# Performance work log

Measured on AMD Instinct MI355X. Metric: run time of the kernel, lower is better.

## Reference

```python
import jax, jax.numpy as jnp
import numpy as np

EPS = 1e-6

def _rms(x, w):
    # RMSNorm over last dim with learned scale w
    var = jnp.mean(x * x, axis=-1, keepdims=True)
    return x * jax.lax.rsqrt(var + EPS) * w

def _split_heads(x, h):
    b, l, hd = x.shape
    return x.reshape(b, l, h, hd // h).transpose(0, 2, 1, 3)  # b h l d

def setup_inputs() -> dict:
    key = jax.random.key(0)
    ks = jax.random.split(key, 12)
    D = 2048          # hidden_size == ip_hidden_states_dim
    H = 16            # n_heads
    Dh = 128          # head_dim
    T = 1280          # timesteps_emb_dim
    B, L, Lip = 2, 2048, 512
    s = 0.02
    return {
        "ip_hidden_states": jax.random.normal(ks[0], (B, Lip, D), jnp.float32),
        "img_query": jax.random.normal(ks[1], (B, L, D), jnp.float32),
        "img_key": jax.random.normal(ks[2], (B, L, D), jnp.float32),
        "img_value": jax.random.normal(ks[3], (B, L, D), jnp.float32),
        "t_emb": jax.random.normal(ks[4], (B, T), jnp.float32),
        "W_ada": jax.random.normal(ks[5], (2 * D, T), jnp.float32) * s,
        "b_ada": jax.random.normal(ks[6], (2 * D,), jnp.float32) * s,
        "W_k_ip": jax.random.normal(ks[7], (D, D), jnp.float32) * s,
        "W_v_ip": jax.random.normal(ks[8], (D, D), jnp.float32) * s,
        "w_q": jnp.ones((Dh,), jnp.float32),
        "w_k": jnp.ones((Dh,), jnp.float32),
        "w_ipk": jnp.ones((Dh,), jnp.float32),
        "n_heads": H,
    }

def reference(ip_hidden_states, img_query, img_key, img_value, t_emb,
              W_ada, b_ada, W_k_ip, W_v_ip, w_q, w_k, w_ipk, n_heads):
    D = img_query.shape[-1]
    # AdaLayerNorm (mode='normal'): silu -> linear -> shift/scale, LN(no affine)
    emb = jax.nn.silu(t_emb) @ W_ada.T + b_ada          # [B, 2D]
    shift, scale = emb[:, :D], emb[:, D:]
    x = ip_hidden_states
    mu = jnp.mean(x, axis=-1, keepdims=True)
    var = jnp.mean((x - mu) ** 2, axis=-1, keepdims=True)
    xn = (x - mu) * jax.lax.rsqrt(var + 1e-6)
    ip_n = xn * (1.0 + scale[:, None, :]) + shift[:, None, :]
    # K/V projections for IP tokens
    ip_key = ip_n @ W_k_ip.T
    ip_value = ip_n @ W_v_ip.T
    # split heads
    q = _split_heads(img_query, n_heads)   # b h L d
    k = _split_heads(img_key, n_heads)
    v = _split_heads(img_value, n_heads)
    kip = _split_heads(ip_key, n_heads)    # b h Lip d
    vip = _split_heads(ip_value, n_heads)
    # RMSNorms
    q = _rms(q, w_q)
    k = _rms(k, w_k)
    kip = _rms(kip, w_ipk)
    # concat image + IP along sequence
    kcat = jnp.concatenate([k, kip], axis=2)
    vcat = jnp.concatenate([v, vip], axis=2)
    # SDPA
    d = q.shape[-1]
    scores = jnp.einsum('bhld,bhmd->bhlm', q, kcat) / jnp.sqrt(jnp.asarray(d, q.dtype))
    attn = jax.nn.softmax(scores, axis=-1)
    out = jnp.einsum('bhlm,bhmd->bhld', attn, vcat)
    b, h, l, dh = out.shape
    return out.transpose(0, 2, 1, 3).reshape(b, l, h * dh)
```

## Files before the change

kernel.cpp:

```cpp
#include <hip/hip_runtime.h>
#include <hip/hip_bf16.h>

typedef __attribute__((ext_vector_type(8))) __bf16 bf16x8;
typedef __attribute__((ext_vector_type(2))) __bf16 bf16x2;
typedef __attribute__((ext_vector_type(4))) float floatx4;
typedef __attribute__((ext_vector_type(4))) short short4v;

#define DEV static __device__ __forceinline__

typedef __attribute__((address_space(1))) const unsigned int gu32;
typedef __attribute__((address_space(3))) unsigned int lu32;

DEV void dma16(const void* g, void* l) {
  __builtin_amdgcn_global_load_lds((gu32*)g, (lu32*)l, 16, 0, 0);
}

DEV unsigned short f2bf(float f) {
  unsigned int u = __float_as_uint(f);
  u += 0x7fffu + ((u >> 16) & 1u);
  return (unsigned short)(u >> 16);
}

DEV unsigned int pk_bf16(float a, float b) {
#if __has_builtin(__builtin_amdgcn_cvt_pk_bf16_f32)
  bf16x2 r = __builtin_amdgcn_cvt_pk_bf16_f32(a, b);
  union { bf16x2 v; unsigned int u; } c; c.v = r;
  return c.u;
#else
  return (unsigned int)f2bf(a) | ((unsigned int)f2bf(b) << 16);
#endif
}

DEV float wred_sum(float v) {
#pragma unroll
  for (int o = 32; o > 0; o >>= 1) v += __shfl_xor(v, o, 64);
  return v;
}

DEV floatx4 mfma32(bf16x8 a, bf16x8 b, floatx4 c) {
  return __builtin_amdgcn_mfma_f32_16x16x32_bf16(a, b, c, 0, 0, 0);
}
DEV floatx4 mfma16(short4v a, short4v b, floatx4 c) {
  return __builtin_amdgcn_mfma_f32_16x16x16bf16_1k(a, b, c, 0, 0, 0);
}

__global__ void ada_kernel(const float* __restrict__ t_emb, const float* __restrict__ W_ada,
                           const float* __restrict__ b_ada, float* __restrict__ emb) {
  int w = threadIdx.x >> 6, lane = threadIdx.x & 63;
  int gid = blockIdx.x * 4 + w;
  int b = gid >> 12, n = gid & 4095;
  const float* te = t_emb + (size_t)b * 1280;
  const float* wr = W_ada + (size_t)n * 1280;
  float acc = 0.f;
#pragma unroll
  for (int i = 0; i < 20; ++i) {
    int t = lane + i * 64;
    float x = te[t];
    float s = x / (1.f + __expf(-x));
    acc += s * wr[t];
  }
  acc = wred_sum(acc);
  if (lane == 0) emb[gid] = acc + b_ada[n];
}

__global__ void ln_mod_kernel(const float* __restrict__ ip, const float* __restrict__ emb,
                              unsigned short* __restrict__ ipn) {
  int row = blockIdx.x;
  int b = row >> 9;
  const float* x = ip + (size_t)row * 2048;
  float xv[8];
  float s1 = 0.f, s2 = 0.f;
#pragma unroll
  for (int i = 0; i < 8; ++i) {
    float v = x[threadIdx.x + i * 256];
    xv[i] = v; s1 += v; s2 += v * v;
  }
  s1 = wred_sum(s1); s2 = wred_sum(s2);
  __shared__ float r1[4], r2[4];
  int w = threadIdx.x >> 6, lane = threadIdx.x & 63;
  if (lane == 0) { r1[w] = s1; r2[w] = s2; }
  __syncthreads();
  s1 = r1[0] + r1[1] + r1[2] + r1[3];
  s2 = r2[0] + r2[1] + r2[2] + r2[3];
  float mu = s1 * (1.f / 2048.f);
  float var = s2 * (1.f / 2048.f) - mu * mu;
  float rs = rsqrtf(var + 1e-6f);
  const float* sh = emb + (size_t)b * 4096;
  unsigned short* y = ipn + (size_t)row * 2048;
#pragma unroll
  for (int i = 0; i < 8; ++i) {
    int d = threadIdx.x + i * 256;
    float v = (xv[i] - mu) * rs;
    v = v * (1.f + sh[2048 + d]) + sh[d];
    y[d] = f2bf(v);
  }
}

struct us4 { unsigned short a, b, c, d; };
__global__ void cvtw_kernel(const float* __restrict__ wk, const float* __restrict__ wv,
                            unsigned short* __restrict__ wk16, unsigned short* __restrict__ wv16) {
  size_t i = ((size_t)blockIdx.x * 256 + threadIdx.x) * 4;
  float4 a = *(const float4*)(wk + i);
  float4 b = *(const float4*)(wv + i);
  us4 oa = { f2bf(a.x), f2bf(a.y), f2bf(a.z), f2bf(a.w) };
  us4 ob = { f2bf(b.x), f2bf(b.y), f2bf(b.z), f2bf(b.w) };
  *(us4*)(wk16 + i) = oa;
  *(us4*)(wv16 + i) = ob;
}

__global__ __launch_bounds__(256) void proj_gemm(const unsigned short* __restrict__ A,
    const unsigned short* __restrict__ Wk, const unsigned short* __restrict__ Wv,
    float* __restrict__ Ck, float* __restrict__ Cv) {
  const unsigned short* Bm = blockIdx.z ? Wv : Wk;
  float* C = blockIdx.z ? Cv : Ck;
  int n0 = blockIdx.x * 64, m0 = blockIdx.y * 128;
  __shared__ __align__(16) unsigned short As[128 * 72];
  __shared__ __align__(16) unsigned short Bs[64 * 72];
  int tid = threadIdx.x, w = tid >> 6, lane = tid & 63, quad = lane >> 4, l16 = lane & 15;
  floatx4 acc[2][4];
#pragma unroll
  for (int i = 0; i < 2; ++i)
#pragma unroll
    for (int j = 0; j < 4; ++j) { floatx4 z = {0.f, 0.f, 0.f, 0.f}; acc[i][j] = z; }
  for (int kk = 0; kk < 2048; kk += 64) {
#pragma unroll
    for (int it = 0; it < 4; ++it) {
      int idx = tid + it * 256;
      int row = idx >> 3, chk = idx & 7;
      *(uint4*)&As[row * 72 + chk * 8] = *(const uint4*)&A[(size_t)(m0 + row) * 2048 + kk + chk * 8];
    }
#pragma unroll
    for (int it = 0; it < 2; ++it) {
      int idx = tid + it * 256;
      int row = idx >> 3, chk = idx & 7;
      *(uint4*)&Bs[row * 72 + chk * 8] = *(const uint4*)&Bm[(size_t)(n0 + row) * 2048 + kk + chk * 8];
    }
    __syncthreads();
#pragma unroll
    for (int c = 0; c < 2; ++c) {
      bf16x8 a0 = *(const bf16x8*)&As[(w * 32 + l16) * 72 + quad * 8 + c * 32];
      bf16x8 a1 = *(const bf16x8*)&As[(w * 32 + 16 + l16) * 72 + quad * 8 + c * 32];
#pragma unroll
      for (int nt = 0; nt < 4; ++nt) {
        bf16x8 bb = *(const bf16x8*)&Bs[(nt * 16 + l16) * 72 + quad * 8 + c * 32];
        acc[0][nt] = mfma32(a0, bb, acc[0][nt]);
        acc[1][nt] = mfma32(a1, bb, acc[1][nt]);
      }
    }
    __syncthreads();
  }
#pragma unroll
  for (int rt = 0; rt < 2; ++rt)
#pragma unroll
    for (int nt = 0; nt < 4; ++nt)
#pragma unroll
      for (int r = 0; r < 4; ++r)
        C[(size_t)(m0 + w * 32 + rt * 16 + quad * 4 + r) * 2048 + n0 + nt * 16 + l16] = acc[rt][nt][r];
}

__global__ __launch_bounds__(256) void kv_build(const float* __restrict__ img_key, const float* __restrict__ img_value,
                         const float* __restrict__ ipk, const float* __restrict__ ipv,
                         const float* __restrict__ w_k, const float* __restrict__ w_ipk,
                         unsigned short* __restrict__ Kc, unsigned short* __restrict__ VtT) {
  int bh = blockIdx.x;
  int mt = blockIdx.y;
  int b = bh >> 4, hh = bh & 15;
  int m0 = mt * 64;
  __shared__ __align__(16) unsigned short Vs[64 * 132];
  int tid = threadIdx.x;
  int mrow = tid >> 2, dq = tid & 3;
  int m = m0 + mrow;
  size_t base;
  const float* wsrc;
  const float *ksrc, *vsrc;
  if (m < 2048) {
    base = (size_t)(b * 2048 + m) * 2048 + hh * 128;
    ksrc = img_key + base; vsrc = img_value + base; wsrc = w_k;
  } else {
    base = (size_t)(b * 512 + (m - 2048)) * 2048 + hh * 128;
    ksrc = ipk + base; vsrc = ipv + base; wsrc = w_ipk;
  }
  float kvv[32]; float ss = 0.f;
  const float4* k4 = (const float4*)ksrc;
#pragma unroll
  for (int i = 0; i < 8; ++i) {
    float4 x = k4[dq * 8 + i];
    kvv[i * 4 + 0] = x.x; kvv[i * 4 + 1] = x.y; kvv[i * 4 + 2] = x.z; kvv[i * 4 + 3] = x.w;
    ss += x.x * x.x + x.y * x.y + x.z * x.z + x.w * x.w;
  }
  ss += __shfl_xor(ss, 1, 64);
  ss += __shfl_xor(ss, 2, 64);
  float rs = rsqrtf(ss * (1.f / 128.f) + 1e-6f);
  unsigned short kb[32];
#pragma unroll
  for (int j = 0; j < 32; ++j) kb[j] = f2bf(kvv[j] * rs * wsrc[dq * 32 + j]);
  uint4* kdst = (uint4*)&Kc[((size_t)bh * 2560 + m) * 128];
#pragma unroll
  for (int i = 0; i < 4; ++i) kdst[(dq * 4 + i) ^ (m & 7)] = ((const uint4*)kb)[i];
  const float4* v4 = (const float4*)vsrc;
#pragma unroll
  for (int i = 0; i < 8; ++i) {
    float4 x = v4[dq * 8 + i];
    us4 p = { f2bf(x.x), f2bf(x.y), f2bf(x.z), f2bf(x.w) };
    *(us4*)&Vs[mrow * 132 + dq * 32 + i * 4] = p;
  }
  __syncthreads();
  int d = tid >> 1, half = tid & 1;
  unsigned short ob[32];
#pragma unroll
  for (int j = 0; j < 32; ++j) ob[j] = Vs[(half * 32 + j) * 132 + d];
  uint4* vdst = (uint4*)&VtT[((size_t)(bh * 40 + mt)) * 8192 + d * 64];
#pragma unroll
  for (int i = 0; i < 4; ++i) vdst[(half * 4 + i) ^ (d & 7)] = ((const uint4*)ob)[i];
}

__global__ __launch_bounds__(256, 3) void attn_kernel(const float* __restrict__ Qf,
    const float* __restrict__ w_q,
    const unsigned short* __restrict__ Kc, const unsigned short* __restrict__ VtT,
    float* __restrict__ out) {
  const float SCL = 0.12751744f;
  const float FM = 17.0f;
  int bh = blockIdx.x & 31;
  int qt = blockIdx.x >> 5;
  int b = bh >> 4, hh = bh & 15;
  int tid = threadIdx.x, w = tid >> 6, lane = tid & 63, quad = lane >> 4, l16 = lane & 15;
  int qh = w >> 1, mh = w & 1;
  int xr = l16 & 7;

  __shared__ __align__(16) unsigned char smem[34048];
  unsigned short* Kt = (unsigned short*)smem;
  unsigned short* Vs = (unsigned short*)(smem + 16384);
  float* epi = (float*)smem;
  __shared__ float rsl[4][32];

  int q0 = qt * 64;

  bf16x8 aq[2][4];
#pragma unroll
  for (int qtl = 0; qtl < 2; ++qtl) {
    int qrow = q0 + qh * 32 + qtl * 16 + l16;
    const float* src = Qf + ((size_t)(b * 2048 + qrow)) * 2048 + hh * 128;
    float xs[32]; float ss = 0.f;
#pragma unroll
    for (int c = 0; c < 4; ++c) {
      float4 a = *(const float4*)&src[quad * 8 + c * 32];
      float4 b2 = *(const float4*)&src[quad * 8 + c * 32 + 4];
      xs[c * 8 + 0] = a.x;  xs[c * 8 + 1] = a.y;  xs[c * 8 + 2] = a.z;  xs[c * 8 + 3] = a.w;
      xs[c * 8 + 4] = b2.x; xs[c * 8 + 5] = b2.y; xs[c * 8 + 6] = b2.z; xs[c * 8 + 7] = b2.w;
      ss += a.x * a.x + a.y * a.y + a.z * a.z + a.w * a.w
          + b2.x * b2.x + b2.y * b2.y + b2.z * b2.z + b2.w * b2.w;
    }
    ss += __shfl_xor(ss, 16, 64);
    ss += __shfl_xor(ss, 32, 64);
    float rs = rsqrtf(ss * (1.f / 128.f) + 1e-6f);
#pragma unroll
    for (int c = 0; c < 4; ++c) {
      float4 wa = *(const float4*)&w_q[quad * 8 + c * 32];
      float4 wb = *(const float4*)&w_q[quad * 8 + c * 32 + 4];
      union { unsigned int u[4]; bf16x8 v; } pk;
      pk.u[0] = pk_bf16(xs[c * 8 + 0] * rs * wa.x, xs[c * 8 + 1] * rs * wa.y);
      pk.u[1] = pk_bf16(xs[c * 8 + 2] * rs * wa.z, xs[c * 8 + 3] * rs * wa.w);
      pk.u[2] = pk_bf16(xs[c * 8 + 4] * rs * wb.x, xs[c * 8 + 5] * rs * wb.y);
      pk.u[3] = pk_bf16(xs[c * 8 + 6] * rs * wb.z, xs[c * 8 + 7] * rs * wb.w);
      aq[qtl][c] = pk.v;
    }
  }

  const unsigned short* Kb = Kc + (size_t)bh * 2560 * 128;
  const unsigned short* Vb = VtT + (size_t)bh * 40 * 8192;

  floatx4 acc[2][8];
#pragma unroll
  for (int i = 0; i < 2; ++i)
#pragma unroll
    for (int j = 0; j < 8; ++j) { floatx4 z = {0.f, 0.f, 0.f, 0.f}; acc[i][j] = z; }
  float rsum[2] = {0.f, 0.f};

  for (int t = 0; t < 40; ++t) {
    const unsigned short* Ksrc = Kb + (size_t)t * 8192;
    const unsigned short* Vsrc = Vb + (size_t)t * 8192;
    int seg = w * 4;
#pragma unroll
    for (int j = 0; j < 4; ++j) {
      int off = (seg + j) * 512 + lane * 8;
      dma16(Ksrc + off, Kt + (seg + j) * 512);
      dma16(Vsrc + off, Vs + (seg + j) * 512);
    }
    __syncthreads();

    short4v pb[2][2];
#pragma unroll
    for (int nt2 = 0; nt2 < 2; ++nt2) {
      floatx4 s0 = {0.f, 0.f, 0.f, 0.f}, s1 = {0.f, 0.f, 0.f, 0.f};
      int krow = (mh * 32 + nt2 * 16 + l16) * 128;
#pragma unroll
      for (int c = 0; c < 4; ++c) {
        bf16x8 bk = *(const bf16x8*)&Kt[krow + ((quad + c * 4) ^ xr) * 8];
        s0 = mfma32(bk, aq[0][c], s0);
        s1 = mfma32(bk, aq[1][c], s1);
      }
      float p0 = __builtin_amdgcn_exp2f(fmaf(s0[0], SCL, -FM));
      float p1 = __builtin_amdgcn_exp2f(fmaf(s0[1], SCL, -FM));
      float p2 = __builtin_amdgcn_exp2f(fmaf(s0[2], SCL, -FM));
      float p3 = __builtin_amdgcn_exp2f(fmaf(s0[3], SCL, -FM));
      rsum[0] += (p0 + p1) + (p2 + p3);
      union { unsigned int u[2]; short4v v; } pa;
      pa.u[0] = pk_bf16(p0, p1); pa.u[1] = pk_bf16(p2, p3);
      pb[nt2][0] = pa.v;
      p0 = __builtin_amdgcn_exp2f(fmaf(s1[0], SCL, -FM));
      p1 = __builtin_amdgcn_exp2f(fmaf(s1[1], SCL, -FM));
      p2 = __builtin_amdgcn_exp2f(fmaf(s1[2], SCL, -FM));
      p3 = __builtin_amdgcn_exp2f(fmaf(s1[3], SCL, -FM));
      rsum[1] += (p0 + p1) + (p2 + p3);
      pa.u[0] = pk_bf16(p0, p1); pa.u[1] = pk_bf16(p2, p3);
      pb[nt2][1] = pa.v;
    }

#pragma unroll
    for (int dt = 0; dt < 8; ++dt) {
      int vrow = (dt * 16 + l16) * 64;
#pragma unroll
      for (int nt2 = 0; nt2 < 2; ++nt2) {
        int mcg = mh * 2 + nt2;
        union { uint2 u; short4v v; } va;
        va.u = *(const uint2*)&Vs[vrow + (((mcg * 2 + (quad >> 1)) ^ xr) * 8) + (quad & 1) * 4];
        acc[0][dt] = mfma16(va.v, pb[nt2][0], acc[0][dt]);
        acc[1][dt] = mfma16(va.v, pb[nt2][1], acc[1][dt]);
      }
    }
    __syncthreads();
  }

  rsum[0] += __shfl_xor(rsum[0], 16, 64); rsum[0] += __shfl_xor(rsum[0], 32, 64);
  rsum[1] += __shfl_xor(rsum[1], 16, 64); rsum[1] += __shfl_xor(rsum[1], 32, 64);
  if (quad == 0) { rsl[w][l16] = rsum[0]; rsl[w][16 + l16] = rsum[1]; }
  if (mh == 1) {
#pragma unroll
    for (int qtl = 0; qtl < 2; ++qtl)
#pragma unroll
      for (int dt = 0; dt < 8; ++dt)
        *(floatx4*)&epi[(qh * 32 + qtl * 16 + l16) * 132 + dt * 16 + quad * 4] = acc[qtl][dt];
  }
  __syncthreads();
  if (mh == 0) {
#pragma unroll
    for (int qtl = 0; qtl < 2; ++qtl) {
      float inv = 1.f / (rsum[qtl] + rsl[w + 1][qtl * 16 + l16]);
      int qrow = q0 + qh * 32 + qtl * 16 + l16;
      float* orow = out + ((size_t)(b * 2048 + qrow)) * 2048 + hh * 128;
#pragma unroll
      for (int dt = 0; dt < 8; ++dt) {
        floatx4 part = *(const floatx4*)&epi[(qh * 32 + qtl * 16 + l16) * 132 + dt * 16 + quad * 4];
        floatx4 r = (acc[qtl][dt] + part) * inv;
        *(floatx4*)&orow[dt * 16 + quad * 4] = r;
      }
    }
  }
}

extern "C" void kernel_launch(void* const* d_in, const int* in_sizes, int n_in,
                              void* d_out, int out_size, void* d_ws, size_t ws_size,
                              hipStream_t stream) {
  const float* ip    = (const float*)d_in[0];
  const float* q     = (const float*)d_in[1];
  const float* k     = (const float*)d_in[2];
  const float* v     = (const float*)d_in[3];
  const float* temb  = (const float*)d_in[4];
  const float* wada  = (const float*)d_in[5];
  const float* bada  = (const float*)d_in[6];
  const float* wkip  = (const float*)d_in[7];
  const float* wvip  = (const float*)d_in[8];
  const float* w_q   = (const float*)d_in[9];
  const float* w_k   = (const float*)d_in[10];
  const float* w_ipk = (const float*)d_in[11];
  float* out = (float*)d_out;
  char* ws = (char*)d_ws;

  float* emb           = (float*)(ws + 0);
  unsigned short* ipn  = (unsigned short*)(ws + 32768);
  unsigned short* wk16 = (unsigned short*)(ws + 4227072);
  unsigned short* wv16 = (unsigned short*)(ws + 12615680);
  unsigned short* Kcat = (unsigned short*)(ws + 16777216);
  unsigned short* VtT  = (unsigned short*)(ws + 37748736);
  float* ipk           = (float*)(ws + 58720256);
  float* ipv           = (float*)(ws + 67108864);

  ada_kernel<<<dim3(2048), dim3(256), 0, stream>>>(temb, wada, bada, emb);
  ln_mod_kernel<<<dim3(1024), dim3(256), 0, stream>>>(ip, emb, ipn);
  cvtw_kernel<<<dim3(4096), dim3(256), 0, stream>>>(wkip, wvip, wk16, wv16);
  proj_gemm<<<dim3(32, 8, 2), dim3(256), 0, stream>>>(ipn, wk16, wv16, ipk, ipv);
  kv_build<<<dim3(32, 40), dim3(256), 0, stream>>>(k, v, ipk, ipv, w_k, w_ipk, Kcat, VtT);
  attn_kernel<<<dim3(1024), dim3(256), 0, stream>>>(q, w_q, Kcat, VtT, out);
}
```

Baseline: 412.3 us.

## Load K fragments directly to registers and double-buffer V tiles in LDS

K is no longer staged through LDS. Each wave loads its K fragments straight from global memory into registers, prefetching the next tile while computing the current one, so the K swizzle in the prep kernel is removed. V tiles are double-buffered in LDS with the DMA for tile t+1 issued before computing tile t, which drops one barrier per iteration. Holding K in registers raises register pressure, so launch bounds fall from 3 to 2 blocks per CU, trading occupancy for overlap. There is a risk of an LDS race because only one barrier per iteration guards reuse of the V buffer.

```diff
diff --git a/kernel.cpp b/kernel.cpp
--- a/kernel.cpp
+++ b/kernel.cpp
@@ -196,7 +196,7 @@
   for (int j = 0; j < 32; ++j) kb[j] = f2bf(kvv[j] * rs * wsrc[dq * 32 + j]);
   uint4* kdst = (uint4*)&Kc[((size_t)bh * 2560 + m) * 128];
 #pragma unroll
-  for (int i = 0; i < 4; ++i) kdst[(dq * 4 + i) ^ (m & 7)] = ((const uint4*)kb)[i];
+  for (int i = 0; i < 4; ++i) kdst[dq * 4 + i] = ((const uint4*)kb)[i];
   const float4* v4 = (const float4*)vsrc;
 #pragma unroll
   for (int i = 0; i < 8; ++i) {
@@ -214,7 +214,7 @@
   for (int i = 0; i < 4; ++i) vdst[(half * 4 + i) ^ (d & 7)] = ((const uint4*)ob)[i];
 }
 
-__global__ __launch_bounds__(256, 3) void attn_kernel(const float* __restrict__ Qf,
+__global__ __launch_bounds__(256, 2) void attn_kernel(const float* __restrict__ Qf,
     const float* __restrict__ w_q,
     const unsigned short* __restrict__ Kc, const unsigned short* __restrict__ VtT,
     float* __restrict__ out) {
@@ -227,11 +227,11 @@
   int qh = w >> 1, mh = w & 1;
   int xr = l16 & 7;
 
-  __shared__ __align__(16) unsigned char smem[34048];
-  unsigned short* Kt = (unsigned short*)smem;
-  unsigned short* Vs = (unsigned short*)(smem + 16384);
+  __shared__ __align__(16) unsigned char smem[34304];
+  unsigned short* Vbuf0 = (unsigned short*)smem;
+  unsigned short* Vbuf1 = (unsigned short*)(smem + 16384);
   float* epi = (float*)smem;
-  __shared__ float rsl[4][32];
+  float* rsl = (float*)(smem + 33792);
 
   int q0 = qt * 64;
 
@@ -269,6 +269,22 @@
   const unsigned short* Kb = Kc + (size_t)bh * 2560 * 128;
   const unsigned short* Vb = VtT + (size_t)bh * 40 * 8192;
 
+  const unsigned short* kp0 = Kb + (size_t)(mh * 32 + l16) * 128 + quad * 8;
+  const unsigned short* kp1 = Kb + (size_t)(mh * 32 + 16 + l16) * 128 + quad * 8;
+
+  bf16x8 kf[2][4], kn[2][4];
+#pragma unroll
+  for (int c = 0; c < 4; ++c) {
+    kf[0][c] = *(const bf16x8*)(kp0 + c * 32);
+    kf[1][c] = *(const bf16x8*)(kp1 + c * 32);
+  }
+  {
+    int seg = w * 4;
+#pragma unroll
+    for (int j = 0; j < 4; ++j)
+      dma16(Vb + (seg + j) * 512 + lane * 8, Vbuf0 + (seg + j) * 512);
+  }
+
   floatx4 acc[2][8];
 #pragma unroll
   for (int i = 0; i < 2; ++i)
@@ -277,27 +293,32 @@
   float rsum[2] = {0.f, 0.f};
 
   for (int t = 0; t < 40; ++t) {
-    const unsigned short* Ksrc = Kb + (size_t)t * 8192;
-    const unsigned short* Vsrc = Vb + (size_t)t * 8192;
-    int seg = w * 4;
-#pragma unroll
-    for (int j = 0; j < 4; ++j) {
-      int off = (seg + j) * 512 + lane * 8;
-      dma16(Ksrc + off, Kt + (seg + j) * 512);
-      dma16(Vsrc + off, Vs + (seg + j) * 512);
-    }
     __syncthreads();
+    unsigned short* Vs = (t & 1) ? Vbuf1 : Vbuf0;
+    if (t < 39) {
+      unsigned short* Vnx = (t & 1) ? Vbuf0 : Vbuf1;
+      const unsigned short* Vsrc = Vb + (size_t)(t + 1) * 8192;
+      int seg = w * 4;
+#pragma unroll
+      for (int j = 0; j < 4; ++j)
+        dma16(Vsrc + (seg + j) * 512 + lane * 8, Vnx + (seg + j) * 512);
+      const unsigned short* k0 = kp0 + (size_t)(t + 1) * 8192;
+      const unsigned short* k1 = kp1 + (size_t)(t + 1) * 8192;
+#pragma unroll
+      for (int c = 0; c < 4; ++c) {
+        kn[0][c] = *(const bf16x8*)(k0 + c * 32);
+        kn[1][c] = *(const bf16x8*)(k1 + c * 32);
+      }
+    }
 
     short4v pb[2][2];
 #pragma unroll
     for (int nt2 = 0; nt2 < 2; ++nt2) {
       floatx4 s0 = {0.f, 0.f, 0.f, 0.f}, s1 = {0.f, 0.f, 0.f, 0.f};
-      int krow = (mh * 32 + nt2 * 16 + l16) * 128;
 #pragma unroll
       for (int c = 0; c < 4; ++c) {
-        bf16x8 bk = *(const bf16x8*)&Kt[krow + ((quad + c * 4) ^ xr) * 8];
-        s0 = mfma32(bk, aq[0][c], s0);
-        s1 = mfma32(bk, aq[1][c], s1);
+        s0 = mfma32(kf[nt2][c], aq[0][c], s0);
+        s1 = mfma32(kf[nt2][c], aq[1][c], s1);
       }
       float p0 = __builtin_amdgcn_exp2f(fmaf(s0[0], SCL, -FM));
       float p1 = __builtin_amdgcn_exp2f(fmaf(s0[1], SCL, -FM));
@@ -328,12 +349,14 @@
         acc[1][dt] = mfma16(va.v, pb[nt2][1], acc[1][dt]);
       }
     }
-    __syncthreads();
-  }
-
+#pragma unroll
+    for (int c = 0; c < 4; ++c) { kf[0][c] = kn[0][c]; kf[1][c] = kn[1][c]; }
+  }
+
+  __syncthreads();
   rsum[0] += __shfl_xor(rsum[0], 16, 64); rsum[0] += __shfl_xor(rsum[0], 32, 64);
   rsum[1] += __shfl_xor(rsum[1], 16, 64); rsum[1] += __shfl_xor(rsum[1], 32, 64);
-  if (quad == 0) { rsl[w][l16] = rsum[0]; rsl[w][16 + l16] = rsum[1]; }
+  if (quad == 0) { rsl[w * 32 + l16] = rsum[0]; rsl[w * 32 + 16 + l16] = rsum[1]; }
   if (mh == 1) {
 #pragma unroll
     for (int qtl = 0; qtl < 2; ++qtl)
@@ -345,7 +368,7 @@
   if (mh == 0) {
 #pragma unroll
     for (int qtl = 0; qtl < 2; ++qtl) {
-      float inv = 1.f / (rsum[qtl] + rsl[w + 1][qtl * 16 + l16]);
+      float inv = 1.f / (rsum[qtl] + rsl[(w + 1) * 32 + qtl * 16 + l16]);
       int qrow = q0 + qh * 32 + qtl * 16 + l16;
       float* orow = out + ((size_t)(b * 2048 + qrow)) * 2048 + hh * 128;
 #pragma unroll
```

After: 485.7 us. +17.8%, slower.
